# Kernel optimization log

Hardware: AMD Instinct MI355X
Metric: run time of the kernel (lower is better)

The kernel has to match this reference:

```python
import jax, jax.numpy as jnp
import numpy as np

K = 16  # hardcoded knn count in Density_loss.forward


def _knn_dist(x, k):
    """Squared pairwise distances [B,N,N], then k smallest per point -> [B,N,k]."""
    sq = jnp.sum(x * x, axis=-1)  # [B,N]
    # d[b,i,j] = |xi|^2 + |xj|^2 - 2 xi.xj
    d = sq[:, :, None] + sq[:, None, :] - 2.0 * jnp.einsum('bic,bjc->bij', x, x)
    neg_topk, _ = jax.lax.top_k(-d, k)  # k smallest distances
    return -neg_topk  # [B,N,k]


def setup_inputs() -> dict:
    key = jax.random.key(0)
    k1, k2 = jax.random.split(key)
    seed = jax.random.normal(k1, (8, 2048, 3), dtype=jnp.float32)
    gt_s = jax.random.normal(k2, (8, 2048, 3), dtype=jnp.float32)
    return {"seed": seed, "gt_s": gt_s}


def reference(seed, gt_s):
    seed_dis = _knn_dist(seed, K).mean(axis=-1)  # [B,N]
    gt_dis = _knn_dist(gt_s, K).mean(axis=-1)    # [B,N]
    # dis_avg=True branch: average over points -> [B], then MSE
    dis = seed_dis.mean(axis=-1)
    gt = gt_dis.mean(axis=-1)
    return jnp.mean((dis - gt) ** 2)
```

## Files before the change

### kernel.cpp

```cpp
#include <hip/hip_runtime.h>
#include <math.h>


#define NPTS 2048
#define KSEL 16
#define WAVES_PER_BLOCK 8
#define BLOCK (WAVES_PER_BLOCK * 64)
#define PTS_PER_BLOCK (WAVES_PER_BLOCK * 2)
#define NGROUPS (NPTS / PTS_PER_BLOCK)
#define NBLOCKS (2 * 8 * NGROUPS)

__device__ __forceinline__ float wave_sum_f(float v) {
  #pragma unroll
  for (int ofs = 32; ofs >= 1; ofs >>= 1) v += __shfl_xor(v, ofs);
  return v;
}

__device__ __forceinline__ float dist2(float px, float py, float pz,
                                       float cx, float cy, float cz) {
  float dx = px - cx, dy = py - cy, dz = pz - cz;
  return fmaf(dz, dz, fmaf(dy, dy, dx * dx));
}

__device__ __forceinline__ float select_sum16(
    const float (&gm)[8], float thr, float px, float py, float pz, int lane,
    const float* xs, const float* ys, const float* zs, int* scrI,
    float* scrV) {
  int qg = 0;
  #pragma unroll
  for (int m = 0; m < 8; ++m) qg += (gm[m] <= thr) ? 1 : 0;
  int incl = qg;
  #pragma unroll
  for (int ofs = 1; ofs < 64; ofs <<= 1) {
    int y = __shfl_up(incl, ofs);
    if (lane >= ofs) incl += y;
  }
  const int tot = __shfl(incl, 63);
  bool ok = (tot <= 64);
  if (ok) {
    int pos = incl - qg;
    #pragma unroll
    for (int m = 0; m < 8; ++m) {
      if (gm[m] <= thr) {
        scrI[pos] = (lane << 3) | m;
        ++pos;
      }
    }
  }

  float d0 = INFINITY, d1 = INFINITY, d2 = INFINITY, d3 = INFINITY;
  if (ok && lane < tot) {
    const int id = scrI[lane];
    const int o = ((id >> 3) << 2) + ((id & 7) << 8);
    float4 cx4 = *(const float4*)&xs[o];
    float4 cy4 = *(const float4*)&ys[o];
    float4 cz4 = *(const float4*)&zs[o];
    d0 = dist2(px, py, pz, cx4.x, cy4.x, cz4.x);
    d1 = dist2(px, py, pz, cx4.y, cy4.y, cz4.y);
    d2 = dist2(px, py, pz, cx4.z, cy4.z, cz4.z);
    d3 = dist2(px, py, pz, cx4.w, cy4.w, cz4.w);
  }

  const int qn = ((d0 <= thr) ? 1 : 0) + ((d1 <= thr) ? 1 : 0) +
                 ((d2 <= thr) ? 1 : 0) + ((d3 <= thr) ? 1 : 0);
  int incl2 = qn;
  #pragma unroll
  for (int ofs = 1; ofs < 64; ofs <<= 1) {
    int y = __shfl_up(incl2, ofs);
    if (lane >= ofs) incl2 += y;
  }
  const int C = __shfl(incl2, 63);
  ok = ok && (C <= 64);

  float res;
  if (ok) {
    int vpos = incl2 - qn;
    if (d0 <= thr) scrV[vpos++] = d0;
    if (d1 <= thr) scrV[vpos++] = d1;
    if (d2 <= thr) scrV[vpos++] = d2;
    if (d3 <= thr) scrV[vpos++] = d3;
    const float v = (lane < C) ? scrV[lane] : INFINITY;

    const unsigned wv = __float_as_uint(v) + 1u;
    unsigned lo = 0u, hi = 0x7F800001u;
    #pragma unroll 1
    for (int r = 0; r < 32; ++r) {
      const unsigned mid = (lo + hi) >> 1;
      const int c = __popcll(__ballot(wv <= mid));
      const bool ge = (c >= KSEL);
      hi = ge ? mid : hi;
      lo = ge ? lo : mid;
    }
    const float tstar = __uint_as_float(hi - 1u);
    const int nlo = __popcll(__ballot(wv <= lo));
    float contrib = (wv <= lo) ? v : 0.f;
    contrib = wave_sum_f(contrib);
    res = contrib + (float)(KSEL - nlo) * tstar;
  } else {
    float s = 0.f;
    unsigned consumed = 0u;
    #pragma unroll 1
    for (int r = 0; r < KSEL; ++r) {
      float bv = INFINITY;
      int bi = 0;
      #pragma unroll
      for (int m = 0; m < 8; ++m) {
        const int o = (lane << 2) + (m << 8);
        float4 cx4 = *(const float4*)&xs[o];
        float4 cy4 = *(const float4*)&ys[o];
        float4 cz4 = *(const float4*)&zs[o];
        float dd;
        bool okb;
        dd = dist2(px, py, pz, cx4.x, cy4.x, cz4.x);
        okb = (((consumed >> ((m << 2) + 0)) & 1u) == 0u) && (dd < bv);
        bv = okb ? dd : bv; bi = okb ? ((m << 2) + 0) : bi;
        dd = dist2(px, py, pz, cx4.y, cy4.y, cz4.y);
        okb = (((consumed >> ((m << 2) + 1)) & 1u) == 0u) && (dd < bv);
        bv = okb ? dd : bv; bi = okb ? ((m << 2) + 1) : bi;
        dd = dist2(px, py, pz, cx4.z, cy4.z, cz4.z);
        okb = (((consumed >> ((m << 2) + 2)) & 1u) == 0u) && (dd < bv);
        bv = okb ? dd : bv; bi = okb ? ((m << 2) + 2) : bi;
        dd = dist2(px, py, pz, cx4.w, cy4.w, cz4.w);
        okb = (((consumed >> ((m << 2) + 3)) & 1u) == 0u) && (dd < bv);
        bv = okb ? dd : bv; bi = okb ? ((m << 2) + 3) : bi;
      }
      int bl = lane;
      #pragma unroll
      for (int ofs = 32; ofs >= 1; ofs >>= 1) {
        float ov = __shfl_xor(bv, ofs);
        int ol = __shfl_xor(bl, ofs);
        bool take = (ov < bv) || (ov == bv && ol < bl);
        bv = take ? ov : bv;
        bl = take ? ol : bl;
      }
      s += bv;
      if (lane == bl) consumed |= (1u << bi);
    }
    res = s;
  }
  return res;
}

__global__ __launch_bounds__(BLOCK) void knn_sum16_kernel(
    const float* __restrict__ seed, const float* __restrict__ gt,
    float* __restrict__ out_sums) {
  __shared__ float xs[NPTS];
  __shared__ float ys[NPTS];
  __shared__ float zs[NPTS];
  __shared__ int scrI[WAVES_PER_BLOCK][2][64];
  __shared__ float scrV[WAVES_PER_BLOCK][2][64];

  const int bid = blockIdx.x;
  const int t = bid >> 10;
  const int b = (bid >> 7) & 7;
  const int g = bid & 127;
  const float* base = (t == 0 ? seed : gt) + b * NPTS * 3;

  const int tid = threadIdx.x;

  {
    const float4* src = (const float4*)base;
    float4 f0 = src[3 * tid + 0];
    float4 f1 = src[3 * tid + 1];
    float4 f2 = src[3 * tid + 2];
    *(float4*)&xs[4 * tid] = make_float4(f0.x, f0.w, f1.z, f2.y);
    *(float4*)&ys[4 * tid] = make_float4(f0.y, f1.x, f1.w, f2.z);
    *(float4*)&zs[4 * tid] = make_float4(f0.z, f1.y, f2.x, f2.w);
  }
  __syncthreads();

  const int wave = tid >> 6;
  const int lane = tid & 63;
  const int iA = g * PTS_PER_BLOCK + wave * 2;
  const int iB = iA + 1;
  const float pax = xs[iA], pay = ys[iA], paz = zs[iA];
  const float pbx = xs[iB], pby = ys[iB], pbz = zs[iB];

  float gmA[8], gmB[8];
  #pragma unroll
  for (int m = 0; m < 8; ++m) {
    const int o = (lane << 2) + (m << 8);
    float4 cx4 = *(const float4*)&xs[o];
    float4 cy4 = *(const float4*)&ys[o];
    float4 cz4 = *(const float4*)&zs[o];
    float a0 = dist2(pax, pay, paz, cx4.x, cy4.x, cz4.x);
    float a1 = dist2(pax, pay, paz, cx4.y, cy4.y, cz4.y);
    float a2 = dist2(pax, pay, paz, cx4.z, cy4.z, cz4.z);
    float a3 = dist2(pax, pay, paz, cx4.w, cy4.w, cz4.w);
    gmA[m] = fminf(fminf(a0, a1), fminf(a2, a3));
    float b0 = dist2(pbx, pby, pbz, cx4.x, cy4.x, cz4.x);
    float b1 = dist2(pbx, pby, pbz, cx4.y, cy4.y, cz4.y);
    float b2 = dist2(pbx, pby, pbz, cx4.z, cy4.z, cz4.z);
    float b3 = dist2(pbx, pby, pbz, cx4.w, cy4.w, cz4.w);
    gmB[m] = fminf(fminf(b0, b1), fminf(b2, b3));
  }
  float lminA = gmA[0], lminB = gmB[0];
  #pragma unroll
  for (int m = 1; m < 8; ++m) {
    lminA = fminf(lminA, gmA[m]);
    lminB = fminf(lminB, gmB[m]);
  }

  const unsigned uA = __float_as_uint(lminA);
  const unsigned uB = __float_as_uint(lminB);
  unsigned loA = 0u, hiA = 0x7F800000u, loB = 0u, hiB = 0x7F800000u;
  #pragma unroll 1
  for (int r = 0; r < 16; ++r) {
    const unsigned midA = (loA + hiA) >> 1;
    const unsigned midB = (loB + hiB) >> 1;
    const int cA = __popcll(__ballot(uA <= midA));
    const int cB = __popcll(__ballot(uB <= midB));
    const bool gA = cA >= KSEL;
    const bool gB = cB >= KSEL;
    hiA = gA ? midA : hiA;
    loA = gA ? loA : midA;
    hiB = gB ? midB : hiB;
    loB = gB ? loB : midB;
  }
  const float thrA = __uint_as_float(hiA);
  const float thrB = __uint_as_float(hiB);

  const float sumA =
      select_sum16(gmA, thrA, pax, pay, paz, lane, xs, ys, zs,
                   &scrI[wave][0][0], &scrV[wave][0][0]);
  const float sumB =
      select_sum16(gmB, thrB, pbx, pby, pbz, lane, xs, ys, zs,
                   &scrI[wave][1][0], &scrV[wave][1][0]);

  if (lane == 0) {
    out_sums[bid * PTS_PER_BLOCK + wave * 2 + 0] = sumA;
    out_sums[bid * PTS_PER_BLOCK + wave * 2 + 1] = sumB;
  }
}

__global__ __launch_bounds__(1024) void final_reduce_kernel(
    const float* __restrict__ sums, float* __restrict__ out) {
  __shared__ float partial[16];
  const int tid = threadIdx.x;
  const int wave = tid >> 6;
  const int lane = tid & 63;
  float s = 0.f;
  #pragma unroll
  for (int m = 0; m < 32; ++m) s += sums[wave * 2048 + lane + (m << 6)];
  #pragma unroll
  for (int ofs = 32; ofs >= 1; ofs >>= 1) s += __shfl_xor(s, ofs);
  if (lane == 0) partial[wave] = s;
  __syncthreads();
  if (tid == 0) {
    const float scale = 1.f / (2048.f * 16.f);
    float acc = 0.f;
    #pragma unroll
    for (int bb = 0; bb < 8; ++bb) {
      float diff = (partial[bb] - partial[8 + bb]) * scale;
      acc += diff * diff;
    }
    out[0] = acc * 0.125f;
  }
}

extern "C" void kernel_launch(void* const* d_in, const int* in_sizes, int n_in,
                              void* d_out, int out_size, void* d_ws, size_t ws_size,
                              hipStream_t stream) {
  const float* seed = (const float*)d_in[0];
  const float* gt = (const float*)d_in[1];
  float* out = (float*)d_out;
  float* ws = (float*)d_ws;

  knn_sum16_kernel<<<NBLOCKS, BLOCK, 0, stream>>>(seed, gt, ws);
  final_reduce_kernel<<<1, 1024, 0, stream>>>(ws, out);
}
```

Measured before the change: 95.45 us.

## Replace scan-compaction top-16 selection with per-lane top-3 and max-peel

The per-point selection no longer compacts candidates through LDS with prefix scans and a 32-step bisection. Each lane now loops only over its qualifying groups, accumulates the sum and count of distances under the threshold, and keeps its three largest. The excess over 16 is then removed by repeatedly peeling the wave-wide maximum. The block also sums its per-point results before writing, so the final reduce reads fewer partials, and the threshold bisection loop is fully unrolled. The exact brute-force fallback still runs when any lane has four or more qualifying candidates, and the new loop's trip count is set by the lane with the most qualifying groups, which can diverge.

```diff
diff --git a/kernel.cpp b/kernel.cpp
--- a/kernel.cpp
+++ b/kernel.cpp
@@ -16,6 +16,12 @@
   return v;
 }
 
+__device__ __forceinline__ float wave_max_f(float v) {
+  #pragma unroll
+  for (int ofs = 32; ofs >= 1; ofs >>= 1) v = fmaxf(v, __shfl_xor(v, ofs));
+  return v;
+}
+
 __device__ __forceinline__ float dist2(float px, float py, float pz,
                                        float cx, float cy, float cz) {
   float dx = px - cx, dy = py - cy, dz = pz - cz;
@@ -24,131 +30,110 @@
 
 __device__ __forceinline__ float select_sum16(
     const float (&gm)[8], float thr, float px, float py, float pz, int lane,
-    const float* xs, const float* ys, const float* zs, int* scrI,
-    float* scrV) {
-  int qg = 0;
-  #pragma unroll
-  for (int m = 0; m < 8; ++m) qg += (gm[m] <= thr) ? 1 : 0;
-  int incl = qg;
-  #pragma unroll
-  for (int ofs = 1; ofs < 64; ofs <<= 1) {
-    int y = __shfl_up(incl, ofs);
-    if (lane >= ofs) incl += y;
-  }
-  const int tot = __shfl(incl, 63);
-  bool ok = (tot <= 64);
-  if (ok) {
-    int pos = incl - qg;
+    const float* xs, const float* ys, const float* zs) {
+  unsigned qmask = 0u;
+  #pragma unroll
+  for (int m = 0; m < 8; ++m) qmask |= (gm[m] <= thr) ? (1u << m) : 0u;
+
+  int qc = 0;
+  float sq = 0.f;
+  float g0 = -INFINITY, g1 = -INFINITY, g2 = -INFINITY;
+  while (__ballot(qmask != 0u) != 0ull) {
+    const bool act = (qmask != 0u);
+    const int m = __ffs(qmask) - 1;
+    qmask &= (qmask - 1u);
+    const int o = act ? ((lane << 2) + (m << 8)) : 0;
+    const float4 cx4 = *(const float4*)&xs[o];
+    const float4 cy4 = *(const float4*)&ys[o];
+    const float4 cz4 = *(const float4*)&zs[o];
+    float dd;
+    #pragma unroll
+    for (int j = 0; j < 4; ++j) {
+      const float cx = (j == 0) ? cx4.x : (j == 1) ? cx4.y : (j == 2) ? cx4.z : cx4.w;
+      const float cy = (j == 0) ? cy4.x : (j == 1) ? cy4.y : (j == 2) ? cy4.z : cy4.w;
+      const float cz = (j == 0) ? cz4.x : (j == 1) ? cz4.y : (j == 2) ? cz4.z : cz4.w;
+      dd = dist2(px, py, pz, cx, cy, cz);
+      const bool q = act && (dd <= thr);
+      const float qd = q ? dd : -INFINITY;
+      qc += q ? 1 : 0;
+      sq += fmaxf(qd, 0.f);
+      const bool c0 = qd > g0;
+      const bool c1 = qd > g1;
+      const float ng2 = c1 ? g1 : fmaxf(g2, qd);
+      const float ng1 = c0 ? g0 : fmaxf(g1, qd);
+      g2 = ng2;
+      g1 = ng1;
+      g0 = fmaxf(g0, qd);
+    }
+  }
+
+  const unsigned long long anyb4 = __ballot(qc >= 4);
+  if (anyb4 == 0ull) {
+    const int C = __popcll(__ballot(qc >= 1)) + __popcll(__ballot(qc >= 2)) +
+                  __popcll(__ballot(qc >= 3));
+    const float S = wave_sum_f(sq);
+    int extras = C - KSEL;
+    float sub = 0.f;
+    while (extras > 0) {
+      const float M = wave_max_f(g0);
+      const unsigned long long sel = __ballot(g0 == M);
+      const int leader = (int)__ffsll(sel) - 1;
+      if (lane == leader) { g0 = g1; g1 = g2; g2 = -INFINITY; }
+      sub += M;
+      --extras;
+    }
+    return S - sub;
+  }
+
+  float s = 0.f;
+  unsigned consumed = 0u;
+  #pragma unroll 1
+  for (int r = 0; r < KSEL; ++r) {
+    float bv = INFINITY;
+    int bi = 0;
     #pragma unroll
     for (int m = 0; m < 8; ++m) {
-      if (gm[m] <= thr) {
-        scrI[pos] = (lane << 3) | m;
-        ++pos;
-      }
-    }
-  }
-
-  float d0 = INFINITY, d1 = INFINITY, d2 = INFINITY, d3 = INFINITY;
-  if (ok && lane < tot) {
-    const int id = scrI[lane];
-    const int o = ((id >> 3) << 2) + ((id & 7) << 8);
-    float4 cx4 = *(const float4*)&xs[o];
-    float4 cy4 = *(const float4*)&ys[o];
-    float4 cz4 = *(const float4*)&zs[o];
-    d0 = dist2(px, py, pz, cx4.x, cy4.x, cz4.x);
-    d1 = dist2(px, py, pz, cx4.y, cy4.y, cz4.y);
-    d2 = dist2(px, py, pz, cx4.z, cy4.z, cz4.z);
-    d3 = dist2(px, py, pz, cx4.w, cy4.w, cz4.w);
-  }
-
-  const int qn = ((d0 <= thr) ? 1 : 0) + ((d1 <= thr) ? 1 : 0) +
-                 ((d2 <= thr) ? 1 : 0) + ((d3 <= thr) ? 1 : 0);
-  int incl2 = qn;
-  #pragma unroll
-  for (int ofs = 1; ofs < 64; ofs <<= 1) {
-    int y = __shfl_up(incl2, ofs);
-    if (lane >= ofs) incl2 += y;
-  }
-  const int C = __shfl(incl2, 63);
-  ok = ok && (C <= 64);
-
-  float res;
-  if (ok) {
-    int vpos = incl2 - qn;
-    if (d0 <= thr) scrV[vpos++] = d0;
-    if (d1 <= thr) scrV[vpos++] = d1;
-    if (d2 <= thr) scrV[vpos++] = d2;
-    if (d3 <= thr) scrV[vpos++] = d3;
-    const float v = (lane < C) ? scrV[lane] : INFINITY;
-
-    const unsigned wv = __float_as_uint(v) + 1u;
-    unsigned lo = 0u, hi = 0x7F800001u;
-    #pragma unroll 1
-    for (int r = 0; r < 32; ++r) {
-      const unsigned mid = (lo + hi) >> 1;
-      const int c = __popcll(__ballot(wv <= mid));
-      const bool ge = (c >= KSEL);
-      hi = ge ? mid : hi;
-      lo = ge ? lo : mid;
-    }
-    const float tstar = __uint_as_float(hi - 1u);
-    const int nlo = __popcll(__ballot(wv <= lo));
-    float contrib = (wv <= lo) ? v : 0.f;
-    contrib = wave_sum_f(contrib);
-    res = contrib + (float)(KSEL - nlo) * tstar;
-  } else {
-    float s = 0.f;
-    unsigned consumed = 0u;
-    #pragma unroll 1
-    for (int r = 0; r < KSEL; ++r) {
-      float bv = INFINITY;
-      int bi = 0;
-      #pragma unroll
-      for (int m = 0; m < 8; ++m) {
-        const int o = (lane << 2) + (m << 8);
-        float4 cx4 = *(const float4*)&xs[o];
-        float4 cy4 = *(const float4*)&ys[o];
-        float4 cz4 = *(const float4*)&zs[o];
-        float dd;
-        bool okb;
-        dd = dist2(px, py, pz, cx4.x, cy4.x, cz4.x);
-        okb = (((consumed >> ((m << 2) + 0)) & 1u) == 0u) && (dd < bv);
-        bv = okb ? dd : bv; bi = okb ? ((m << 2) + 0) : bi;
-        dd = dist2(px, py, pz, cx4.y, cy4.y, cz4.y);
-        okb = (((consumed >> ((m << 2) + 1)) & 1u) == 0u) && (dd < bv);
-        bv = okb ? dd : bv; bi = okb ? ((m << 2) + 1) : bi;
-        dd = dist2(px, py, pz, cx4.z, cy4.z, cz4.z);
-        okb = (((consumed >> ((m << 2) + 2)) & 1u) == 0u) && (dd < bv);
-        bv = okb ? dd : bv; bi = okb ? ((m << 2) + 2) : bi;
-        dd = dist2(px, py, pz, cx4.w, cy4.w, cz4.w);
-        okb = (((consumed >> ((m << 2) + 3)) & 1u) == 0u) && (dd < bv);
-        bv = okb ? dd : bv; bi = okb ? ((m << 2) + 3) : bi;
-      }
-      int bl = lane;
-      #pragma unroll
-      for (int ofs = 32; ofs >= 1; ofs >>= 1) {
-        float ov = __shfl_xor(bv, ofs);
-        int ol = __shfl_xor(bl, ofs);
-        bool take = (ov < bv) || (ov == bv && ol < bl);
-        bv = take ? ov : bv;
-        bl = take ? ol : bl;
-      }
-      s += bv;
-      if (lane == bl) consumed |= (1u << bi);
-    }
-    res = s;
-  }
-  return res;
+      const int o = (lane << 2) + (m << 8);
+      const float4 cx4 = *(const float4*)&xs[o];
+      const float4 cy4 = *(const float4*)&ys[o];
+      const float4 cz4 = *(const float4*)&zs[o];
+      float dd;
+      bool okb;
+      dd = dist2(px, py, pz, cx4.x, cy4.x, cz4.x);
+      okb = (((consumed >> ((m << 2) + 0)) & 1u) == 0u) && (dd < bv);
+      bv = okb ? dd : bv; bi = okb ? ((m << 2) + 0) : bi;
+      dd = dist2(px, py, pz, cx4.y, cy4.y, cz4.y);
+      okb = (((consumed >> ((m << 2) + 1)) & 1u) == 0u) && (dd < bv);
+      bv = okb ? dd : bv; bi = okb ? ((m << 2) + 1) : bi;
+      dd = dist2(px, py, pz, cx4.z, cy4.z, cz4.z);
+      okb = (((consumed >> ((m << 2) + 2)) & 1u) == 0u) && (dd < bv);
+      bv = okb ? dd : bv; bi = okb ? ((m << 2) + 2) : bi;
+      dd = dist2(px, py, pz, cx4.w, cy4.w, cz4.w);
+      okb = (((consumed >> ((m << 2) + 3)) & 1u) == 0u) && (dd < bv);
+      bv = okb ? dd : bv; bi = okb ? ((m << 2) + 3) : bi;
+    }
+    int bl = lane;
+    #pragma unroll
+    for (int ofs = 32; ofs >= 1; ofs >>= 1) {
+      float ov = __shfl_xor(bv, ofs);
+      int ol = __shfl_xor(bl, ofs);
+      bool take = (ov < bv) || (ov == bv && ol < bl);
+      bv = take ? ov : bv;
+      bl = take ? ol : bl;
+    }
+    s += bv;
+    if (lane == bl) consumed |= (1u << bi);
+  }
+  return s;
 }
 
 __global__ __launch_bounds__(BLOCK) void knn_sum16_kernel(
     const float* __restrict__ seed, const float* __restrict__ gt,
-    float* __restrict__ out_sums) {
+    float* __restrict__ out_part) {
   __shared__ float xs[NPTS];
   __shared__ float ys[NPTS];
   __shared__ float zs[NPTS];
-  __shared__ int scrI[WAVES_PER_BLOCK][2][64];
-  __shared__ float scrV[WAVES_PER_BLOCK][2][64];
+  __shared__ float bsums[WAVES_PER_BLOCK];
 
   const int bid = blockIdx.x;
   const int t = bid >> 10;
@@ -180,9 +165,9 @@
   #pragma unroll
   for (int m = 0; m < 8; ++m) {
     const int o = (lane << 2) + (m << 8);
-    float4 cx4 = *(const float4*)&xs[o];
-    float4 cy4 = *(const float4*)&ys[o];
-    float4 cz4 = *(const float4*)&zs[o];
+    const float4 cx4 = *(const float4*)&xs[o];
+    const float4 cy4 = *(const float4*)&ys[o];
+    const float4 cz4 = *(const float4*)&zs[o];
     float a0 = dist2(pax, pay, paz, cx4.x, cy4.x, cz4.x);
     float a1 = dist2(pax, pay, paz, cx4.y, cy4.y, cz4.y);
     float a2 = dist2(pax, pay, paz, cx4.z, cy4.z, cz4.z);
@@ -204,7 +189,7 @@
   const unsigned uA = __float_as_uint(lminA);
   const unsigned uB = __float_as_uint(lminB);
   unsigned loA = 0u, hiA = 0x7F800000u, loB = 0u, hiB = 0x7F800000u;
-  #pragma unroll 1
+  #pragma unroll
   for (int r = 0; r < 16; ++r) {
     const unsigned midA = (loA + hiA) >> 1;
     const unsigned midB = (loB + hiB) >> 1;
@@ -220,28 +205,26 @@
   const float thrA = __uint_as_float(hiA);
   const float thrB = __uint_as_float(hiB);
 
-  const float sumA =
-      select_sum16(gmA, thrA, pax, pay, paz, lane, xs, ys, zs,
-                   &scrI[wave][0][0], &scrV[wave][0][0]);
-  const float sumB =
-      select_sum16(gmB, thrB, pbx, pby, pbz, lane, xs, ys, zs,
-                   &scrI[wave][1][0], &scrV[wave][1][0]);
-
-  if (lane == 0) {
-    out_sums[bid * PTS_PER_BLOCK + wave * 2 + 0] = sumA;
-    out_sums[bid * PTS_PER_BLOCK + wave * 2 + 1] = sumB;
+  const float sumA = select_sum16(gmA, thrA, pax, pay, paz, lane, xs, ys, zs);
+  const float sumB = select_sum16(gmB, thrB, pbx, pby, pbz, lane, xs, ys, zs);
+
+  if (lane == 0) bsums[wave] = sumA + sumB;
+  __syncthreads();
+  if (tid == 0) {
+    float s = 0.f;
+    #pragma unroll
+    for (int w = 0; w < WAVES_PER_BLOCK; ++w) s += bsums[w];
+    out_part[bid] = s;
   }
 }
 
 __global__ __launch_bounds__(1024) void final_reduce_kernel(
-    const float* __restrict__ sums, float* __restrict__ out) {
+    const float* __restrict__ parts, float* __restrict__ out) {
   __shared__ float partial[16];
   const int tid = threadIdx.x;
   const int wave = tid >> 6;
   const int lane = tid & 63;
-  float s = 0.f;
-  #pragma unroll
-  for (int m = 0; m < 32; ++m) s += sums[wave * 2048 + lane + (m << 6)];
+  float s = parts[wave * NGROUPS + lane] + parts[wave * NGROUPS + 64 + lane];
   #pragma unroll
   for (int ofs = 32; ofs >= 1; ofs >>= 1) s += __shfl_xor(s, ofs);
   if (lane == 0) partial[wave] = s;
```

Result: slower. 127.2 us (+33.3%).
